# Performance work log

Measured on AMD Instinct MI355X. Metric: run time of the kernel, lower is better.

The kernel has to match this reference:

```python
import jax, jax.numpy as jnp
import numpy as np

B, L, D = 2, 1024, 512
E = 2
DI = E * D            # d_inner = 1024
N = 16                # d_state
K = 4                 # d_conv
DT_RANK = 32          # ceil(d_model / 16)


def setup_inputs() -> dict:
    key = jax.random.key(0)
    ks = jax.random.split(key, 12)
    s = lambda i, shape, scale=0.02: jax.random.normal(ks[i], shape, jnp.float32) * scale
    return {
        "x": jax.random.normal(ks[0], (B, L, D), jnp.float32),
        # Mamba params (mamba_ssm layout: Linear weights are [out, in])
        "W_in": s(1, (2 * DI, D)),                 # in_proj, bias=False
        "conv_w": s(2, (DI, K), 0.1),              # depthwise conv kernel
        "conv_b": jnp.zeros((DI,), jnp.float32),
        "W_xproj": s(3, (DT_RANK + 2 * N, DI)),    # x_proj, bias=False
        "W_dt": s(4, (DI, DT_RANK), 0.1),
        "b_dt": s(5, (DI,), 0.5),
        "A_log": jnp.log(jnp.broadcast_to(jnp.arange(1, N + 1, dtype=jnp.float32), (DI, N))),
        "D_skip": jnp.ones((DI,), jnp.float32),
        "W_out": s(6, (D, DI)),                    # out_proj, bias=False
        # block params
        "g1": jnp.ones((D,), jnp.float32), "b1": jnp.zeros((D,), jnp.float32),
        "W_ff1": s(7, (2 * D, D)), "b_ff1": jnp.zeros((2 * D,), jnp.float32),
        "W_ff2": s(8, (D, 2 * D)), "b_ff2": jnp.zeros((D,), jnp.float32),
        "g2": jnp.ones((D,), jnp.float32), "b2": jnp.zeros((D,), jnp.float32),
    }


def layernorm(x, g, b, eps=1e-5):
    m = x.mean(-1, keepdims=True)
    v = jnp.mean(jnp.square(x - m), -1, keepdims=True)
    return (x - m) * jax.lax.rsqrt(v + eps) * g + b


def mamba(x, W_in, conv_w, conv_b, W_xproj, W_dt, b_dt, A_log, D_skip, W_out):
    xz = x @ W_in.T                              # [B,L,2*DI]
    u, z = jnp.split(xz, 2, axis=-1)             # each [B,L,DI]
    # causal depthwise conv1d over time
    u_t = u.transpose(0, 2, 1)                   # [B,DI,L]
    conv = jax.lax.conv_general_dilated(
        u_t, conv_w[:, None, :], (1,), [(K - 1, 0)], feature_group_count=DI)
    u = jax.nn.silu(conv.transpose(0, 2, 1) + conv_b)   # [B,L,DI]
    # input-dependent dt, B, C
    x_dbl = u @ W_xproj.T                        # [B,L,DT_RANK+2N]
    dt_r, Bm, Cm = jnp.split(x_dbl, [DT_RANK, DT_RANK + N], axis=-1)
    dt = jax.nn.softplus(dt_r @ W_dt.T + b_dt)   # [B,L,DI]
    A = -jnp.exp(A_log)                          # [DI,N]
    dA = jnp.exp(dt[..., None] * A)                                # [B,L,DI,N]
    dBu = dt[..., None] * Bm[:, :, None, :] * u[..., None]         # [B,L,DI,N]

    def step(h, xs):
        dA_t, dBu_t, C_t = xs
        h = dA_t * h + dBu_t                    # [B,DI,N]
        y = jnp.einsum('bdn,bn->bd', h, C_t)
        return h, y

    h0 = jnp.zeros((B, DI, N), dt.dtype)
    _, ys = jax.lax.scan(step, h0, (dA.transpose(1, 0, 2, 3),
                                    dBu.transpose(1, 0, 2, 3),
                                    Cm.transpose(1, 0, 2)))
    y = ys.transpose(1, 0, 2) + u * D_skip       # [B,L,DI]
    y = y * jax.nn.silu(z)
    return y @ W_out.T                            # [B,L,D]


def reference(x, W_in, conv_w, conv_b, W_xproj, W_dt, b_dt, A_log, D_skip, W_out,
              g1, b1, W_ff1, b_ff1, W_ff2, b_ff2, g2, b2):
    m = mamba(x, W_in, conv_w, conv_b, W_xproj, W_dt, b_dt, A_log, D_skip, W_out)
    res1 = x - m
    r = layernorm(res1, g1, b1)
    ff = jax.nn.gelu(r @ W_ff1.T + b_ff1, approximate=False) @ W_ff2.T + b_ff2
    res2 = r - ff
    out = layernorm(jax.nn.silu(res2), g2, b2)
    return out + x
```

## Files before the change

### kernel.cpp

```cpp
#include <hip/hip_runtime.h>
#include <math.h>

#define BB 2
#define LL 1024
#define DD 512
#define DIN 1024
#define NS 16
#define RNK 32
#define ML (BB*LL)
#define CT 16
#define NC (LL/CT)
#define BDIN (BB*DIN)

typedef unsigned short u16;
typedef unsigned int u32;

__device__ __forceinline__ float sigmoidf_(float v) { return 1.f / (1.f + __expf(-v)); }
__device__ __forceinline__ float siluf_(float v) { return v * sigmoidf_(v); }
__device__ __forceinline__ u16 f2bf(float f) {
  union { float f; u32 u; } c; c.f = f;
  u32 r = c.u + 0x7fffu + ((c.u >> 16) & 1u);
  return (u16)(r >> 16);
}
__device__ __forceinline__ float bf2f(u16 x) {
  union { u32 u; float f; } c; c.u = (u32)x << 16;
  return c.f;
}

__global__ __launch_bounds__(256) void cast_all(const float* __restrict__ x,
                                                const float* __restrict__ Wi,
                                                const float* __restrict__ Wx,
                                                const float* __restrict__ Wd,
                                                const float* __restrict__ Wo,
                                                const float* __restrict__ Wf1,
                                                const float* __restrict__ Wf2,
                                                u16* bx, u16* bWi, u16* bWx, u16* bWd,
                                                u16* bWo, u16* bWf1, u16* bWf2)
{
  int bid = blockIdx.x;
  const float* src; u16* dst; int base;
  if (bid < 512)       { src = x;   dst = bx;   base = 0; }
  else if (bid < 1024) { src = Wi;  dst = bWi;  base = 512; }
  else if (bid < 1056) { src = Wx;  dst = bWx;  base = 1024; }
  else if (bid < 1072) { src = Wd;  dst = bWd;  base = 1056; }
  else if (bid < 1328) { src = Wo;  dst = bWo;  base = 1072; }
  else if (bid < 1584) { src = Wf1; dst = bWf1; base = 1328; }
  else                 { src = Wf2; dst = bWf2; base = 1584; }
  int i = ((bid - base) * 256 + threadIdx.x) * 8;
  float4 v0 = *(const float4*)&src[i];
  float4 v1 = *(const float4*)&src[i + 4];
  union { u16 u[8]; uint4 v; } p;
  p.u[0] = f2bf(v0.x); p.u[1] = f2bf(v0.y); p.u[2] = f2bf(v0.z); p.u[3] = f2bf(v0.w);
  p.u[4] = f2bf(v1.x); p.u[5] = f2bf(v1.y); p.u[6] = f2bf(v1.z); p.u[7] = f2bf(v1.w);
  *(uint4*)&dst[i] = p.v;
}

using bf16x8 = __attribute__((ext_vector_type(8))) short;
using f32x4  = __attribute__((ext_vector_type(4))) float;

template<int BM, int BN, int EPI, typename OT>
__global__ __launch_bounds__(256) void gemm_t(const u16* __restrict__ A,
                                              const u16* __restrict__ W,
                                              const float* __restrict__ bias,
                                              OT* __restrict__ C,
                                              int M, int N, int K)
{
  constexpr int WR = BM / 64;
  constexpr int WC = 4 / WR;
  constexpr int NW = BN / WC;
  constexpr int JJ = NW / 16;
  constexpr int RB = BN / 64;
  __shared__ u16 As[BM][40];
  __shared__ u16 Bs[BN][40];
  const int bm = blockIdx.y * BM, bn = blockIdx.x * BN;
  const int tid = threadIdx.x;
  const int w = tid >> 6, l = tid & 63;
  const int wr = w / WC, wc = w % WC;
  const int lr = l & 15, lh = l >> 4;
  const int sr0 = tid >> 2, sc0 = tid & 3;
  f32x4 acc[4][JJ] = {};
  for (int k0 = 0; k0 < K; k0 += 32) {
    uint4 areg[WR], breg[RB];
#pragma unroll
    for (int i = 0; i < WR; ++i)
      areg[i] = *(const uint4*)&A[(size_t)(bm + sr0 + 64 * i) * K + k0 + sc0 * 8];
#pragma unroll
    for (int i = 0; i < RB; ++i)
      breg[i] = *(const uint4*)&W[(size_t)(bn + sr0 + 64 * i) * K + k0 + sc0 * 8];
    __syncthreads();
#pragma unroll
    for (int i = 0; i < WR; ++i) *(uint4*)&As[sr0 + 64 * i][sc0 * 8] = areg[i];
#pragma unroll
    for (int i = 0; i < RB; ++i) *(uint4*)&Bs[sr0 + 64 * i][sc0 * 8] = breg[i];
    __syncthreads();
    bf16x8 af[4], bfr[JJ];
#pragma unroll
    for (int i = 0; i < 4; ++i) af[i]  = *(bf16x8*)&As[wr * 64 + i * 16 + lr][lh * 8];
#pragma unroll
    for (int j = 0; j < JJ; ++j) bfr[j] = *(bf16x8*)&Bs[wc * NW + j * 16 + lr][lh * 8];
#pragma unroll
    for (int i = 0; i < 4; ++i)
#pragma unroll
      for (int j = 0; j < JJ; ++j)
        acc[i][j] = __builtin_amdgcn_mfma_f32_16x16x32_bf16(af[i], bfr[j], acc[i][j], 0, 0, 0);
  }
#pragma unroll
  for (int i = 0; i < 4; ++i) {
#pragma unroll
    for (int j = 0; j < JJ; ++j) {
      int col = bn + wc * NW + j * 16 + lr;
      float bv = (EPI >= 1) ? bias[col] : 0.f;
#pragma unroll
      for (int r = 0; r < 4; ++r) {
        int row = bm + wr * 64 + i * 16 + lh * 4 + r;
        float t = acc[i][j][r] + bv;
        if (EPI == 2) t = 0.5f * t * (1.f + erff(t * 0.70710678118654752f));
        if (EPI == 3) t = fmaxf(t, 0.f) + log1pf(__expf(-fabsf(t)));
        if constexpr (sizeof(OT) == 2) C[(size_t)row * N + col] = (OT)f2bf(t);
        else                           C[(size_t)row * N + col] = (OT)t;
      }
    }
  }
}

__global__ __launch_bounds__(256) void xproj_mfma(const u16* __restrict__ A,
                                                  const u16* __restrict__ W,
                                                  float* __restrict__ C,
                                                  u16* __restrict__ bdtr)
{
  __shared__ u16 As[128][40];
  __shared__ u16 Bs[64][40];
  const int bm = blockIdx.x * 128;
  const int tid = threadIdx.x;
  const int w = tid >> 6, l = tid & 63;
  const int lr = l & 15, lh = l >> 4;
  const int sr0 = tid >> 2, sc0 = tid & 3;
  f32x4 acc[2][4] = {};
  for (int k0 = 0; k0 < DIN; k0 += 32) {
    uint4 a0 = *(const uint4*)&A[(size_t)(bm + sr0) * DIN + k0 + sc0 * 8];
    uint4 a1 = *(const uint4*)&A[(size_t)(bm + sr0 + 64) * DIN + k0 + sc0 * 8];
    uint4 b0;
    if (sr0 < 64) b0 = *(const uint4*)&W[(size_t)sr0 * DIN + k0 + sc0 * 8];
    __syncthreads();
    *(uint4*)&As[sr0][sc0 * 8] = a0;
    *(uint4*)&As[sr0 + 64][sc0 * 8] = a1;
    if (sr0 < 64) *(uint4*)&Bs[sr0][sc0 * 8] = b0;
    __syncthreads();
    bf16x8 af[2], bfr[4];
#pragma unroll
    for (int i = 0; i < 2; ++i) af[i]  = *(bf16x8*)&As[w * 32 + i * 16 + lr][lh * 8];
#pragma unroll
    for (int j = 0; j < 4; ++j) bfr[j] = *(bf16x8*)&Bs[j * 16 + lr][lh * 8];
#pragma unroll
    for (int i = 0; i < 2; ++i)
#pragma unroll
      for (int j = 0; j < 4; ++j)
        acc[i][j] = __builtin_amdgcn_mfma_f32_16x16x32_bf16(af[i], bfr[j], acc[i][j], 0, 0, 0);
  }
#pragma unroll
  for (int i = 0; i < 2; ++i)
#pragma unroll
    for (int j = 0; j < 4; ++j) {
      int col = j * 16 + lr;
#pragma unroll
      for (int r = 0; r < 4; ++r) {
        int row = bm + w * 32 + i * 16 + lh * 4 + r;
        float v = acc[i][j][r];
        C[(size_t)row * 64 + col] = v;
        if (j < 2) bdtr[(size_t)row * RNK + col] = f2bf(v);
      }
    }
}

__global__ __launch_bounds__(256) void conv_silu(const u16* __restrict__ xzb,
                                                 const float* __restrict__ conv_w,
                                                 const float* __restrict__ conv_b,
                                                 u16* __restrict__ ucb)
{
  int idx = blockIdx.x * 256 + threadIdx.x;
  int d = idx & (DIN - 1);
  int bl = idx >> 10;
  int l = bl & (LL - 1);
  int b = bl >> 10;
  float acc = conv_b[d];
#pragma unroll
  for (int k = 0; k < 4; ++k) {
    int ls = l - 3 + k;
    float uv = (ls >= 0) ? bf2f(xzb[((size_t)(b * LL + ls)) * (2 * DIN) + d]) : 0.f;
    acc = fmaf(uv, conv_w[d * 4 + k], acc);
  }
  ucb[idx] = f2bf(siluf_(acc));
}


__global__ __launch_bounds__(256) void scan_p1(const float* __restrict__ dt,
                                               const u16* __restrict__ ucb,
                                               const float* __restrict__ xdbl,
                                               const float* __restrict__ A_log,
                                               float* __restrict__ apG,
                                               float* __restrict__ hG)
{
  __shared__ float dts[CT][256];
  __shared__ float us[CT][256];
  __shared__ float Bs[CT][NS];
  const int d0 = blockIdx.x * 256, c = blockIdx.y, b = blockIdx.z;
  const int tid = threadIdx.x;
  const int t0 = c * CT;
  for (int i = tid; i < CT * 64; i += 256) {
    int r = i >> 6, col = (i & 63) * 4;
    size_t row = (size_t)(b * LL + t0 + r);
    *(float4*)&dts[r][col] = *(const float4*)&dt[row * DIN + d0 + col];
    ushort4 uv = *(const ushort4*)&ucb[row * DIN + d0 + col];
    float4 uf = { bf2f(uv.x), bf2f(uv.y), bf2f(uv.z), bf2f(uv.w) };
    *(float4*)&us[r][col] = uf;
  }
  { int r = tid >> 4, n = tid & 15;
    Bs[r][n] = xdbl[(size_t)(b * LL + t0 + r) * 64 + 32 + n]; }
  __syncthreads();
  const int d = d0 + tid;
  float Ad[NS];
#pragma unroll
  for (int n = 0; n < NS; ++n) Ad[n] = -__expf(A_log[d * NS + n]);
  float h[NS] = {};
  float sdt = 0.f;
#pragma unroll 4
  for (int t = 0; t < CT; ++t) {
    float dtv = dts[t][tid];
    float dtu = dtv * us[t][tid];
    sdt += dtv;
    float4 B0 = *(float4*)&Bs[t][0],  B1 = *(float4*)&Bs[t][4];
    float4 B2 = *(float4*)&Bs[t][8],  B3 = *(float4*)&Bs[t][12];
    float Bq[NS] = { B0.x, B0.y, B0.z, B0.w, B1.x, B1.y, B1.z, B1.w,
                     B2.x, B2.y, B2.z, B2.w, B3.x, B3.y, B3.z, B3.w };
#pragma unroll
    for (int n = 0; n < NS; ++n) {
      float a = __expf(dtv * Ad[n]);
      h[n] = fmaf(a, h[n], dtu * Bq[n]);
    }
  }
  const int bd = b * DIN + d;
#pragma unroll
  for (int n = 0; n < NS; ++n) {
    apG[((size_t)c * NS + n) * BDIN + bd] = __expf(Ad[n] * sdt);
    hG [((size_t)c * NS + n) * BDIN + bd] = h[n];
  }
}

__global__ __launch_bounds__(128) void scan_p2(const float* __restrict__ apG,
                                               float* __restrict__ hG)
{
  const int idx = blockIdx.x * 128 + threadIdx.x;
  float H = 0.f;
#pragma unroll 16
  for (int c = 0; c < NC; ++c) {
    size_t o = (size_t)c * (NS * BDIN) + idx;
    float ap = apG[o];
    float hl = hG[o];
    hG[o] = H;
    H = fmaf(ap, H, hl);
  }
}

__global__ __launch_bounds__(256) void scan_p3(const float* __restrict__ dt,
                                               const u16* __restrict__ ucb,
                                               const u16* __restrict__ xzb,
                                               const float* __restrict__ xdbl,
                                               const float* __restrict__ A_log,
                                               const float* __restrict__ D_skip,
                                               const float* __restrict__ hG,
                                               u16* __restrict__ ygb)
{
  __shared__ float dts[CT][256];
  __shared__ float us[CT][256];
  __shared__ float zs[CT][256];
  __shared__ float Bs[CT][NS];
  __shared__ float Cs[CT][NS];
  const int d0 = blockIdx.x * 256, c = blockIdx.y, b = blockIdx.z;
  const int tid = threadIdx.x;
  const int t0 = c * CT;
  for (int i = tid; i < CT * 64; i += 256) {
    int r = i >> 6, col = (i & 63) * 4;
    size_t row = (size_t)(b * LL + t0 + r);
    *(float4*)&dts[r][col] = *(const float4*)&dt[row * DIN + d0 + col];
    ushort4 uv = *(const ushort4*)&ucb[row * DIN + d0 + col];
    float4 uf = { bf2f(uv.x), bf2f(uv.y), bf2f(uv.z), bf2f(uv.w) };
    *(float4*)&us[r][col] = uf;
    ushort4 zv = *(const ushort4*)&xzb[row * (2 * DIN) + DIN + d0 + col];
    float4 zf = { bf2f(zv.x), bf2f(zv.y), bf2f(zv.z), bf2f(zv.w) };
    *(float4*)&zs[r][col] = zf;
  }
  { int r = tid >> 4, n = tid & 15;
    size_t row = (size_t)(b * LL + t0 + r);
    Bs[r][n] = xdbl[row * 64 + 32 + n];
    Cs[r][n] = xdbl[row * 64 + 48 + n]; }
  __syncthreads();
  const int d = d0 + tid;
  const int bd = b * DIN + d;
  float Ad[NS];
#pragma unroll
  for (int n = 0; n < NS; ++n) Ad[n] = -__expf(A_log[d * NS + n]);
  const float Dd = D_skip[d];
  float h[NS];
#pragma unroll
  for (int n = 0; n < NS; ++n) h[n] = hG[((size_t)c * NS + n) * BDIN + bd];
#pragma unroll 2
  for (int t = 0; t < CT; ++t) {
    float dtv = dts[t][tid];
    float ucv = us[t][tid];
    float dtu = dtv * ucv;
    float4 B0 = *(float4*)&Bs[t][0],  B1 = *(float4*)&Bs[t][4];
    float4 B2 = *(float4*)&Bs[t][8],  B3 = *(float4*)&Bs[t][12];
    float4 C0 = *(float4*)&Cs[t][0],  C1 = *(float4*)&Cs[t][4];
    float4 C2 = *(float4*)&Cs[t][8],  C3 = *(float4*)&Cs[t][12];
    float Bq[NS] = { B0.x, B0.y, B0.z, B0.w, B1.x, B1.y, B1.z, B1.w,
                     B2.x, B2.y, B2.z, B2.w, B3.x, B3.y, B3.z, B3.w };
    float Cq[NS] = { C0.x, C0.y, C0.z, C0.w, C1.x, C1.y, C1.z, C1.w,
                     C2.x, C2.y, C2.z, C2.w, C3.x, C3.y, C3.z, C3.w };
    float y = 0.f;
#pragma unroll
    for (int n = 0; n < NS; ++n) {
      float a = __expf(dtv * Ad[n]);
      h[n] = fmaf(a, h[n], dtu * Bq[n]);
      y = fmaf(h[n], Cq[n], y);
    }
    float o = fmaf(ucv, Dd, y) * siluf_(zs[t][tid]);
    ygb[(size_t)(b * LL + t0 + t) * DIN + d0 + tid] = f2bf(o);
  }
}

__global__ __launch_bounds__(256) void ln1_kernel(const float* __restrict__ x,
                                                  const float* __restrict__ m,
                                                  const float* __restrict__ g,
                                                  const float* __restrict__ b,
                                                  float* __restrict__ r,
                                                  u16* __restrict__ rbf)
{
  int row = blockIdx.x;
  int tid = threadIdx.x;
  size_t base = (size_t)row * DD;
  float2 xv = *(const float2*)&x[base + tid * 2];
  float2 mv = *(const float2*)&m[base + tid * 2];
  float v0 = xv.x - mv.x, v1 = xv.y - mv.y;
  float s = v0 + v1, ss = v0 * v0 + v1 * v1;
#pragma unroll
  for (int off = 32; off; off >>= 1) { s += __shfl_down(s, off, 64); ss += __shfl_down(ss, off, 64); }
  __shared__ float sm[8];
  int w = tid >> 6;
  if ((tid & 63) == 0) { sm[w] = s; sm[4 + w] = ss; }
  __syncthreads();
  float S = sm[0] + sm[1] + sm[2] + sm[3];
  float SS = sm[4] + sm[5] + sm[6] + sm[7];
  float mean = S * (1.f / DD);
  float var = SS * (1.f / DD) - mean * mean;
  float rstd = rsqrtf(var + 1e-5f);
  float2 gv = *(const float2*)&g[tid * 2];
  float2 bv = *(const float2*)&b[tid * 2];
  float2 o;
  o.x = (v0 - mean) * rstd * gv.x + bv.x;
  o.y = (v1 - mean) * rstd * gv.y + bv.y;
  *(float2*)&r[base + tid * 2] = o;
  u32 pk = (u32)f2bf(o.x) | ((u32)f2bf(o.y) << 16);
  *(u32*)&rbf[base + tid * 2] = pk;
}

__global__ __launch_bounds__(256) void final_kernel(const float* __restrict__ r,
                                                    const float* __restrict__ ff,
                                                    const float* __restrict__ x,
                                                    const float* __restrict__ g,
                                                    const float* __restrict__ b,
                                                    float* __restrict__ out)
{
  int row = blockIdx.x;
  int tid = threadIdx.x;
  size_t base = (size_t)row * DD;
  float2 rv = *(const float2*)&r[base + tid * 2];
  float2 fv = *(const float2*)&ff[base + tid * 2];
  float v0 = rv.x - fv.x, v1 = rv.y - fv.y;
  v0 = siluf_(v0); v1 = siluf_(v1);
  float s = v0 + v1, ss = v0 * v0 + v1 * v1;
#pragma unroll
  for (int off = 32; off; off >>= 1) { s += __shfl_down(s, off, 64); ss += __shfl_down(ss, off, 64); }
  __shared__ float sm[8];
  int w = tid >> 6;
  if ((tid & 63) == 0) { sm[w] = s; sm[4 + w] = ss; }
  __syncthreads();
  float S = sm[0] + sm[1] + sm[2] + sm[3];
  float SS = sm[4] + sm[5] + sm[6] + sm[7];
  float mean = S * (1.f / DD);
  float var = SS * (1.f / DD) - mean * mean;
  float rstd = rsqrtf(var + 1e-5f);
  float2 gv = *(const float2*)&g[tid * 2];
  float2 bv = *(const float2*)&b[tid * 2];
  float2 xv = *(const float2*)&x[base + tid * 2];
  float2 o;
  o.x = (v0 - mean) * rstd * gv.x + bv.x + xv.x;
  o.y = (v1 - mean) * rstd * gv.y + bv.y + xv.y;
  *(float2*)&out[base + tid * 2] = o;
}

extern "C" void kernel_launch(void* const* d_in, const int* in_sizes, int n_in,
                              void* d_out, int out_size, void* d_ws, size_t ws_size,
                              hipStream_t stream)
{
  const float* x      = (const float*)d_in[0];
  const float* W_in   = (const float*)d_in[1];
  const float* conv_w = (const float*)d_in[2];
  const float* conv_b = (const float*)d_in[3];
  const float* W_xp   = (const float*)d_in[4];
  const float* W_dt   = (const float*)d_in[5];
  const float* b_dt   = (const float*)d_in[6];
  const float* A_log  = (const float*)d_in[7];
  const float* D_skip = (const float*)d_in[8];
  const float* W_out  = (const float*)d_in[9];
  const float* g1     = (const float*)d_in[10];
  const float* b1     = (const float*)d_in[11];
  const float* W_ff1  = (const float*)d_in[12];
  const float* b_ff1  = (const float*)d_in[13];
  const float* W_ff2  = (const float*)d_in[14];
  const float* b_ff2  = (const float*)d_in[15];
  const float* g2     = (const float*)d_in[16];
  const float* b2     = (const float*)d_in[17];
  float* out = (float*)d_out;

  float* ws = (float*)d_ws;
  u16*   xzb    = (u16*)ws;
  float* xdbl   = ws + 4194304;
  float* dtb    = ws + 4325376;
  float* apG    = ws + 6422528;
  float* hG     = ws + 8519680;
  float* mb     = ws + 10616832;
  float* rb     = ws + 11665408;
  u16*   bffh   = (u16*)(ws + 12713984);
  u16*   ygb    = (u16*)(ws + 13762560);
  u16*   ucb    = (u16*)(ws + 14811136);
  u16*   brb    = (u16*)(ws + 15859712);
  u16*   bdtr   = (u16*)(ws + 16384000);
  u16*   bx     = (u16*)(ws + 16416768);
  u16*   bW_in  = (u16*)(ws + 16941056);
  u16*   bWxp   = (u16*)(ws + 17989632);
  u16*   bW_dt  = (u16*)(ws + 18022400);
  u16*   bW_out = (u16*)(ws + 18038784);
  u16*   bW_ff1 = (u16*)(ws + 18300928);
  u16*   bW_ff2 = (u16*)(ws + 18563072);

  cast_all<<<1840, 256, 0, stream>>>(x, W_in, W_xp, W_dt, W_out, W_ff1, W_ff2,
                                     bx, bW_in, bWxp, bW_dt, bW_out, bW_ff1, bW_ff2);
  gemm_t<128, 64, 0, u16><<<dim3(2 * DIN / 64, ML / 128), 256, 0, stream>>>(
      bx, bW_in, nullptr, xzb, ML, 2 * DIN, DD);
  conv_silu<<<(ML * DIN) / 256, 256, 0, stream>>>(xzb, conv_w, conv_b, ucb);
  xproj_mfma<<<ML / 128, 256, 0, stream>>>(ucb, bWxp, xdbl, bdtr);
  gemm_t<128, 64, 3, float><<<dim3(DIN / 64, ML / 128), 256, 0, stream>>>(
      bdtr, bW_dt, b_dt, dtb, ML, DIN, RNK);
  scan_p1<<<dim3(DIN / 256, NC, BB), 256, 0, stream>>>(dtb, ucb, xdbl, A_log, apG, hG);
  scan_p2<<<(NS * BDIN) / 128, 128, 0, stream>>>(apG, hG);
  scan_p3<<<dim3(DIN / 256, NC, BB), 256, 0, stream>>>(dtb, ucb, xzb, xdbl, A_log, D_skip,
                                                       hG, ygb);
  gemm_t<64, 64, 0, float><<<dim3(DD / 64, ML / 64), 256, 0, stream>>>(
      ygb, bW_out, nullptr, mb, ML, DD, DIN);
  ln1_kernel<<<ML, 256, 0, stream>>>(x, mb, g1, b1, rb, brb);
  gemm_t<128, 64, 2, u16><<<dim3(DIN / 64, ML / 128), 256, 0, stream>>>(
      brb, bW_ff1, b_ff1, bffh, ML, DIN, DD);
  gemm_t<64, 64, 1, float><<<dim3(DD / 64, ML / 64), 256, 0, stream>>>(
      bffh, bW_ff2, b_ff2, mb, ML, DD, DIN);
  final_kernel<<<ML, 256, 0, stream>>>(rb, mb, x, g2, b2, out);
}
```

Before: 174.0 us.

## Fuse out_proj and FF2 GEMMs with layernorm epilogues; store dt as bf16

Replaces the out_proj GEMM plus ln1 kernel and the FF2 GEMM plus final kernel with a single full-row GEMM kernel (64 rows x 512 cols per block) that computes the residual, layernorm statistics via shuffles and shared memory, and writes normalized output directly. This removes the intermediate fp32 buffer round trips and two launches. It also stores dt in bf16 to halve its traffic in the scan kernels. The fused GEMM launches only 32 blocks, which risks severe underutilization of the GPU, and bf16 dt reduces precision.

After: 351.4 us. 102% more time.

```diff
diff --git a/kernel.cpp b/kernel.cpp
--- a/kernel.cpp
+++ b/kernel.cpp
@@ -123,6 +123,110 @@
   }
 }
 
+template<int MODE>
+__global__ __launch_bounds__(256) void gemm_ln(const u16* __restrict__ A,
+                                               const u16* __restrict__ W,
+                                               const float* __restrict__ bias,
+                                               const float* __restrict__ xres,
+                                               const float* __restrict__ rln,
+                                               const float* __restrict__ g,
+                                               const float* __restrict__ b,
+                                               float* __restrict__ outF,
+                                               u16* __restrict__ outB)
+{
+  constexpr int K = DIN;
+  __shared__ u16 As[64][40];
+  __shared__ u16 Bs[512][40];
+  __shared__ float red[64][8];
+  const int bm = blockIdx.x * 64;
+  const int tid = threadIdx.x;
+  const int wv = tid >> 6, l = tid & 63;
+  const int lr = l & 15, lh = l >> 4;
+  const int sr0 = tid >> 2, sc0 = tid & 3;
+  f32x4 acc[4][8] = {};
+  for (int k0 = 0; k0 < K; k0 += 32) {
+    uint4 areg = *(const uint4*)&A[(size_t)(bm + sr0) * K + k0 + sc0 * 8];
+    uint4 breg[8];
+#pragma unroll
+    for (int i = 0; i < 8; ++i)
+      breg[i] = *(const uint4*)&W[(size_t)(sr0 + 64 * i) * K + k0 + sc0 * 8];
+    __syncthreads();
+    *(uint4*)&As[sr0][sc0 * 8] = areg;
+#pragma unroll
+    for (int i = 0; i < 8; ++i) *(uint4*)&Bs[sr0 + 64 * i][sc0 * 8] = breg[i];
+    __syncthreads();
+    bf16x8 af[4], bfr[8];
+#pragma unroll
+    for (int i = 0; i < 4; ++i) af[i]  = *(bf16x8*)&As[i * 16 + lr][lh * 8];
+#pragma unroll
+    for (int j = 0; j < 8; ++j) bfr[j] = *(bf16x8*)&Bs[wv * 128 + j * 16 + lr][lh * 8];
+#pragma unroll
+    for (int i = 0; i < 4; ++i)
+#pragma unroll
+      for (int j = 0; j < 8; ++j)
+        acc[i][j] = __builtin_amdgcn_mfma_f32_16x16x32_bf16(af[i], bfr[j], acc[i][j], 0, 0, 0);
+  }
+#pragma unroll
+  for (int i = 0; i < 4; ++i)
+#pragma unroll
+    for (int j = 0; j < 8; ++j) {
+      int col = wv * 128 + j * 16 + lr;
+#pragma unroll
+      for (int r = 0; r < 4; ++r) {
+        int row = bm + i * 16 + lh * 4 + r;
+        float a = acc[i][j][r];
+        float v;
+        if (MODE == 0) {
+          v = xres[(size_t)row * DD + col] - a;
+        } else {
+          float ff = a + bias[col];
+          v = siluf_(rln[(size_t)row * DD + col] - ff);
+        }
+        acc[i][j][r] = v;
+      }
+    }
+#pragma unroll
+  for (int i = 0; i < 4; ++i)
+#pragma unroll
+    for (int r = 0; r < 4; ++r) {
+      float s = 0.f, ss = 0.f;
+#pragma unroll
+      for (int j = 0; j < 8; ++j) {
+        float v = acc[i][j][r];
+        s += v; ss += v * v;
+      }
+      s  += __shfl_xor(s, 1, 16);  ss += __shfl_xor(ss, 1, 16);
+      s  += __shfl_xor(s, 2, 16);  ss += __shfl_xor(ss, 2, 16);
+      s  += __shfl_xor(s, 4, 16);  ss += __shfl_xor(ss, 4, 16);
+      s  += __shfl_xor(s, 8, 16);  ss += __shfl_xor(ss, 8, 16);
+      if (lr == 0) { red[i * 16 + lh * 4 + r][wv * 2] = s; red[i * 16 + lh * 4 + r][wv * 2 + 1] = ss; }
+    }
+  __syncthreads();
+#pragma unroll
+  for (int i = 0; i < 4; ++i)
+#pragma unroll
+    for (int r = 0; r < 4; ++r) {
+      int rlcl = i * 16 + lh * 4 + r;
+      int row = bm + rlcl;
+      float S  = red[rlcl][0] + red[rlcl][2] + red[rlcl][4] + red[rlcl][6];
+      float SS = red[rlcl][1] + red[rlcl][3] + red[rlcl][5] + red[rlcl][7];
+      float mean = S * (1.f / DD);
+      float var = SS * (1.f / DD) - mean * mean;
+      float rstd = rsqrtf(var + 1e-5f);
+#pragma unroll
+      for (int j = 0; j < 8; ++j) {
+        int col = wv * 128 + j * 16 + lr;
+        float vn = (acc[i][j][r] - mean) * rstd * g[col] + b[col];
+        if (MODE == 0) {
+          outF[(size_t)row * DD + col] = vn;
+          outB[(size_t)row * DD + col] = f2bf(vn);
+        } else {
+          outF[(size_t)row * DD + col] = vn + xres[(size_t)row * DD + col];
+        }
+      }
+    }
+}
+
 __global__ __launch_bounds__(256) void xproj_mfma(const u16* __restrict__ A,
                                                   const u16* __restrict__ W,
                                                   float* __restrict__ C,
@@ -193,7 +297,7 @@
 }
 
 
-__global__ __launch_bounds__(256) void scan_p1(const float* __restrict__ dt,
+__global__ __launch_bounds__(256) void scan_p1(const u16* __restrict__ dtb,
                                                const u16* __restrict__ ucb,
                                                const float* __restrict__ xdbl,
                                                const float* __restrict__ A_log,
@@ -209,7 +313,9 @@
   for (int i = tid; i < CT * 64; i += 256) {
     int r = i >> 6, col = (i & 63) * 4;
     size_t row = (size_t)(b * LL + t0 + r);
-    *(float4*)&dts[r][col] = *(const float4*)&dt[row * DIN + d0 + col];
+    ushort4 dv = *(const ushort4*)&dtb[row * DIN + d0 + col];
+    float4 df = { bf2f(dv.x), bf2f(dv.y), bf2f(dv.z), bf2f(dv.w) };
+    *(float4*)&dts[r][col] = df;
     ushort4 uv = *(const ushort4*)&ucb[row * DIN + d0 + col];
     float4 uf = { bf2f(uv.x), bf2f(uv.y), bf2f(uv.z), bf2f(uv.w) };
     *(float4*)&us[r][col] = uf;
@@ -261,7 +367,7 @@
   }
 }
 
-__global__ __launch_bounds__(256) void scan_p3(const float* __restrict__ dt,
+__global__ __launch_bounds__(256) void scan_p3(const u16* __restrict__ dtb,
                                                const u16* __restrict__ ucb,
                                                const u16* __restrict__ xzb,
                                                const float* __restrict__ xdbl,
@@ -281,7 +387,9 @@
   for (int i = tid; i < CT * 64; i += 256) {
     int r = i >> 6, col = (i & 63) * 4;
     size_t row = (size_t)(b * LL + t0 + r);
-    *(float4*)&dts[r][col] = *(const float4*)&dt[row * DIN + d0 + col];
+    ushort4 dv = *(const ushort4*)&dtb[row * DIN + d0 + col];
+    float4 df = { bf2f(dv.x), bf2f(dv.y), bf2f(dv.z), bf2f(dv.w) };
+    *(float4*)&dts[r][col] = df;
     ushort4 uv = *(const ushort4*)&ucb[row * DIN + d0 + col];
     float4 uf = { bf2f(uv.x), bf2f(uv.y), bf2f(uv.z), bf2f(uv.w) };
     *(float4*)&us[r][col] = uf;
@@ -326,76 +434,6 @@
     float o = fmaf(ucv, Dd, y) * siluf_(zs[t][tid]);
     ygb[(size_t)(b * LL + t0 + t) * DIN + d0 + tid] = f2bf(o);
   }
-}
-
-__global__ __launch_bounds__(256) void ln1_kernel(const float* __restrict__ x,
-                                                  const float* __restrict__ m,
-                                                  const float* __restrict__ g,
-                                                  const float* __restrict__ b,
-                                                  float* __restrict__ r,
-                                                  u16* __restrict__ rbf)
-{
-  int row = blockIdx.x;
-  int tid = threadIdx.x;
-  size_t base = (size_t)row * DD;
-  float2 xv = *(const float2*)&x[base + tid * 2];
-  float2 mv = *(const float2*)&m[base + tid * 2];
-  float v0 = xv.x - mv.x, v1 = xv.y - mv.y;
-  float s = v0 + v1, ss = v0 * v0 + v1 * v1;
-#pragma unroll
-  for (int off = 32; off; off >>= 1) { s += __shfl_down(s, off, 64); ss += __shfl_down(ss, off, 64); }
-  __shared__ float sm[8];
-  int w = tid >> 6;
-  if ((tid & 63) == 0) { sm[w] = s; sm[4 + w] = ss; }
-  __syncthreads();
-  float S = sm[0] + sm[1] + sm[2] + sm[3];
-  float SS = sm[4] + sm[5] + sm[6] + sm[7];
-  float mean = S * (1.f / DD);
-  float var = SS * (1.f / DD) - mean * mean;
-  float rstd = rsqrtf(var + 1e-5f);
-  float2 gv = *(const float2*)&g[tid * 2];
-  float2 bv = *(const float2*)&b[tid * 2];
-  float2 o;
-  o.x = (v0 - mean) * rstd * gv.x + bv.x;
-  o.y = (v1 - mean) * rstd * gv.y + bv.y;
-  *(float2*)&r[base + tid * 2] = o;
-  u32 pk = (u32)f2bf(o.x) | ((u32)f2bf(o.y) << 16);
-  *(u32*)&rbf[base + tid * 2] = pk;
-}
-
-__global__ __launch_bounds__(256) void final_kernel(const float* __restrict__ r,
-                                                    const float* __restrict__ ff,
-                                                    const float* __restrict__ x,
-                                                    const float* __restrict__ g,
-                                                    const float* __restrict__ b,
-                                                    float* __restrict__ out)
-{
-  int row = blockIdx.x;
-  int tid = threadIdx.x;
-  size_t base = (size_t)row * DD;
-  float2 rv = *(const float2*)&r[base + tid * 2];
-  float2 fv = *(const float2*)&ff[base + tid * 2];
-  float v0 = rv.x - fv.x, v1 = rv.y - fv.y;
-  v0 = siluf_(v0); v1 = siluf_(v1);
-  float s = v0 + v1, ss = v0 * v0 + v1 * v1;
-#pragma unroll
-  for (int off = 32; off; off >>= 1) { s += __shfl_down(s, off, 64); ss += __shfl_down(ss, off, 64); }
-  __shared__ float sm[8];
-  int w = tid >> 6;
-  if ((tid & 63) == 0) { sm[w] = s; sm[4 + w] = ss; }
-  __syncthreads();
-  float S = sm[0] + sm[1] + sm[2] + sm[3];
-  float SS = sm[4] + sm[5] + sm[6] + sm[7];
-  float mean = S * (1.f / DD);
-  float var = SS * (1.f / DD) - mean * mean;
-  float rstd = rsqrtf(var + 1e-5f);
-  float2 gv = *(const float2*)&g[tid * 2];
-  float2 bv = *(const float2*)&b[tid * 2];
-  float2 xv = *(const float2*)&x[base + tid * 2];
-  float2 o;
-  o.x = (v0 - mean) * rstd * gv.x + bv.x + xv.x;
-  o.y = (v1 - mean) * rstd * gv.y + bv.y + xv.y;
-  *(float2*)&out[base + tid * 2] = o;
 }
 
 extern "C" void kernel_launch(void* const* d_in, const int* in_sizes, int n_in,
@@ -425,10 +463,9 @@
   float* ws = (float*)d_ws;
   u16*   xzb    = (u16*)ws;
   float* xdbl   = ws + 4194304;
-  float* dtb    = ws + 4325376;
+  u16*   dtb    = (u16*)(ws + 4325376);
   float* apG    = ws + 6422528;
   float* hG     = ws + 8519680;
-  float* mb     = ws + 10616832;
   float* rb     = ws + 11665408;
   u16*   bffh   = (u16*)(ws + 12713984);
   u16*   ygb    = (u16*)(ws + 13762560);
@@ -449,18 +486,14 @@
       bx, bW_in, nullptr, xzb, ML, 2 * DIN, DD);
   conv_silu<<<(ML * DIN) / 256, 256, 0, stream>>>(xzb, conv_w, conv_b, ucb);
   xproj_mfma<<<ML / 128, 256, 0, stream>>>(ucb, bWxp, xdbl, bdtr);
-  gemm_t<128, 64, 3, float><<<dim3(DIN / 64, ML / 128), 256, 0, stream>>>(
+  gemm_t<128, 64, 3, u16><<<dim3(DIN / 64, ML / 128), 256, 0, stream>>>(
       bdtr, bW_dt, b_dt, dtb, ML, DIN, RNK);
   scan_p1<<<dim3(DIN / 256, NC, BB), 256, 0, stream>>>(dtb, ucb, xdbl, A_log, apG, hG);
   scan_p2<<<(NS * BDIN) / 128, 128, 0, stream>>>(apG, hG);
   scan_p3<<<dim3(DIN / 256, NC, BB), 256, 0, stream>>>(dtb, ucb, xzb, xdbl, A_log, D_skip,
                                                        hG, ygb);
-  gemm_t<64, 64, 0, float><<<dim3(DD / 64, ML / 64), 256, 0, stream>>>(
-      ygb, bW_out, nullptr, mb, ML, DD, DIN);
-  ln1_kernel<<<ML, 256, 0, stream>>>(x, mb, g1, b1, rb, brb);
+  gemm_ln<0><<<ML / 64, 256, 0, stream>>>(ygb, bW_out, nullptr, x, nullptr, g1, b1, rb, brb);
   gemm_t<128, 64, 2, u16><<<dim3(DIN / 64, ML / 128), 256, 0, stream>>>(
       brb, bW_ff1, b_ff1, bffh, ML, DIN, DD);
-  gemm_t<64, 64, 1, float><<<dim3(DD / 64, ML / 64), 256, 0, stream>>>(
-      bffh, bW_ff2, b_ff2, mb, ML, DD, DIN);
-  final_kernel<<<ML, 256, 0, stream>>>(rb, mb, x, g2, b2, out);
-}
+  gemm_ln<1><<<ML / 64, 256, 0, stream>>>(bffh, bW_ff2, b_ff2, x, rb, g2, b2, out, nullptr);
+}
```

## Fuse fp32-to-bf16 casts into GEMM loads and store dt as bf16

Applied to the files above, without the earlier changes.

Removes the standalone cast_all kernel and converts x and the weights from fp32 to bf16 inside each GEMM's global load path through a templated ld8bf helper. The dt softplus output is now stored as bf16 rather than fp32, so the scan kernels read half as many bytes for dt. This saves a kernel launch and a write/read round trip for the casted buffers. In exchange, weights are re-read as fp32 and re-converted by every block tile that touches them, and dt loses precision.

Result: no change. 174.9 us (+0.5%).

```diff
diff --git a/kernel.cpp b/kernel.cpp
--- a/kernel.cpp
+++ b/kernel.cpp
@@ -27,40 +27,26 @@
   return c.f;
 }
 
-__global__ __launch_bounds__(256) void cast_all(const float* __restrict__ x,
-                                                const float* __restrict__ Wi,
-                                                const float* __restrict__ Wx,
-                                                const float* __restrict__ Wd,
-                                                const float* __restrict__ Wo,
-                                                const float* __restrict__ Wf1,
-                                                const float* __restrict__ Wf2,
-                                                u16* bx, u16* bWi, u16* bWx, u16* bWd,
-                                                u16* bWo, u16* bWf1, u16* bWf2)
-{
-  int bid = blockIdx.x;
-  const float* src; u16* dst; int base;
-  if (bid < 512)       { src = x;   dst = bx;   base = 0; }
-  else if (bid < 1024) { src = Wi;  dst = bWi;  base = 512; }
-  else if (bid < 1056) { src = Wx;  dst = bWx;  base = 1024; }
-  else if (bid < 1072) { src = Wd;  dst = bWd;  base = 1056; }
-  else if (bid < 1328) { src = Wo;  dst = bWo;  base = 1072; }
-  else if (bid < 1584) { src = Wf1; dst = bWf1; base = 1328; }
-  else                 { src = Wf2; dst = bWf2; base = 1584; }
-  int i = ((bid - base) * 256 + threadIdx.x) * 8;
-  float4 v0 = *(const float4*)&src[i];
-  float4 v1 = *(const float4*)&src[i + 4];
-  union { u16 u[8]; uint4 v; } p;
-  p.u[0] = f2bf(v0.x); p.u[1] = f2bf(v0.y); p.u[2] = f2bf(v0.z); p.u[3] = f2bf(v0.w);
-  p.u[4] = f2bf(v1.x); p.u[5] = f2bf(v1.y); p.u[6] = f2bf(v1.z); p.u[7] = f2bf(v1.w);
-  *(uint4*)&dst[i] = p.v;
+template<typename T>
+__device__ __forceinline__ uint4 ld8bf(const T* p);
+template<> __device__ __forceinline__ uint4 ld8bf<u16>(const u16* p) {
+  return *(const uint4*)p;
+}
+template<> __device__ __forceinline__ uint4 ld8bf<float>(const float* p) {
+  float4 v0 = *(const float4*)p;
+  float4 v1 = *(const float4*)(p + 4);
+  union { u16 u[8]; uint4 v; } q;
+  q.u[0] = f2bf(v0.x); q.u[1] = f2bf(v0.y); q.u[2] = f2bf(v0.z); q.u[3] = f2bf(v0.w);
+  q.u[4] = f2bf(v1.x); q.u[5] = f2bf(v1.y); q.u[6] = f2bf(v1.z); q.u[7] = f2bf(v1.w);
+  return q.v;
 }
 
 using bf16x8 = __attribute__((ext_vector_type(8))) short;
 using f32x4  = __attribute__((ext_vector_type(4))) float;
 
-template<int BM, int BN, int EPI, typename OT>
-__global__ __launch_bounds__(256) void gemm_t(const u16* __restrict__ A,
-                                              const u16* __restrict__ W,
+template<int BM, int BN, int EPI, typename OT, typename TA, typename TW>
+__global__ __launch_bounds__(256) void gemm_t(const TA* __restrict__ A,
+                                              const TW* __restrict__ W,
                                               const float* __restrict__ bias,
                                               OT* __restrict__ C,
                                               int M, int N, int K)
@@ -83,10 +69,10 @@
     uint4 areg[WR], breg[RB];
 #pragma unroll
     for (int i = 0; i < WR; ++i)
-      areg[i] = *(const uint4*)&A[(size_t)(bm + sr0 + 64 * i) * K + k0 + sc0 * 8];
+      areg[i] = ld8bf(&A[(size_t)(bm + sr0 + 64 * i) * K + k0 + sc0 * 8]);
 #pragma unroll
     for (int i = 0; i < RB; ++i)
-      breg[i] = *(const uint4*)&W[(size_t)(bn + sr0 + 64 * i) * K + k0 + sc0 * 8];
+      breg[i] = ld8bf(&W[(size_t)(bn + sr0 + 64 * i) * K + k0 + sc0 * 8]);
     __syncthreads();
 #pragma unroll
     for (int i = 0; i < WR; ++i) *(uint4*)&As[sr0 + 64 * i][sc0 * 8] = areg[i];
@@ -124,7 +110,7 @@
 }
 
 __global__ __launch_bounds__(256) void xproj_mfma(const u16* __restrict__ A,
-                                                  const u16* __restrict__ W,
+                                                  const float* __restrict__ W,
                                                   float* __restrict__ C,
                                                   u16* __restrict__ bdtr)
 {
@@ -137,10 +123,10 @@
   const int sr0 = tid >> 2, sc0 = tid & 3;
   f32x4 acc[2][4] = {};
   for (int k0 = 0; k0 < DIN; k0 += 32) {
-    uint4 a0 = *(const uint4*)&A[(size_t)(bm + sr0) * DIN + k0 + sc0 * 8];
-    uint4 a1 = *(const uint4*)&A[(size_t)(bm + sr0 + 64) * DIN + k0 + sc0 * 8];
+    uint4 a0 = ld8bf(&A[(size_t)(bm + sr0) * DIN + k0 + sc0 * 8]);
+    uint4 a1 = ld8bf(&A[(size_t)(bm + sr0 + 64) * DIN + k0 + sc0 * 8]);
     uint4 b0;
-    if (sr0 < 64) b0 = *(const uint4*)&W[(size_t)sr0 * DIN + k0 + sc0 * 8];
+    if (sr0 < 64) b0 = ld8bf(&W[(size_t)sr0 * DIN + k0 + sc0 * 8]);
     __syncthreads();
     *(uint4*)&As[sr0][sc0 * 8] = a0;
     *(uint4*)&As[sr0 + 64][sc0 * 8] = a1;
@@ -193,7 +179,7 @@
 }
 
 
-__global__ __launch_bounds__(256) void scan_p1(const float* __restrict__ dt,
+__global__ __launch_bounds__(256) void scan_p1(const u16* __restrict__ dtb,
                                                const u16* __restrict__ ucb,
                                                const float* __restrict__ xdbl,
                                                const float* __restrict__ A_log,
@@ -209,7 +195,9 @@
   for (int i = tid; i < CT * 64; i += 256) {
     int r = i >> 6, col = (i & 63) * 4;
     size_t row = (size_t)(b * LL + t0 + r);
-    *(float4*)&dts[r][col] = *(const float4*)&dt[row * DIN + d0 + col];
+    ushort4 dv = *(const ushort4*)&dtb[row * DIN + d0 + col];
+    float4 df = { bf2f(dv.x), bf2f(dv.y), bf2f(dv.z), bf2f(dv.w) };
+    *(float4*)&dts[r][col] = df;
     ushort4 uv = *(const ushort4*)&ucb[row * DIN + d0 + col];
     float4 uf = { bf2f(uv.x), bf2f(uv.y), bf2f(uv.z), bf2f(uv.w) };
     *(float4*)&us[r][col] = uf;
@@ -261,7 +249,7 @@
   }
 }
 
-__global__ __launch_bounds__(256) void scan_p3(const float* __restrict__ dt,
+__global__ __launch_bounds__(256) void scan_p3(const u16* __restrict__ dtb,
                                                const u16* __restrict__ ucb,
                                                const u16* __restrict__ xzb,
                                                const float* __restrict__ xdbl,
@@ -281,7 +269,9 @@
   for (int i = tid; i < CT * 64; i += 256) {
     int r = i >> 6, col = (i & 63) * 4;
     size_t row = (size_t)(b * LL + t0 + r);
-    *(float4*)&dts[r][col] = *(const float4*)&dt[row * DIN + d0 + col];
+    ushort4 dv = *(const ushort4*)&dtb[row * DIN + d0 + col];
+    float4 df = { bf2f(dv.x), bf2f(dv.y), bf2f(dv.z), bf2f(dv.w) };
+    *(float4*)&dts[r][col] = df;
     ushort4 uv = *(const ushort4*)&ucb[row * DIN + d0 + col];
     float4 uf = { bf2f(uv.x), bf2f(uv.y), bf2f(uv.z), bf2f(uv.w) };
     *(float4*)&us[r][col] = uf;
@@ -423,44 +413,35 @@
   float* out = (float*)d_out;
 
   float* ws = (float*)d_ws;
-  u16*   xzb    = (u16*)ws;
-  float* xdbl   = ws + 4194304;
-  float* dtb    = ws + 4325376;
-  float* apG    = ws + 6422528;
-  float* hG     = ws + 8519680;
-  float* mb     = ws + 10616832;
-  float* rb     = ws + 11665408;
-  u16*   bffh   = (u16*)(ws + 12713984);
-  u16*   ygb    = (u16*)(ws + 13762560);
-  u16*   ucb    = (u16*)(ws + 14811136);
-  u16*   brb    = (u16*)(ws + 15859712);
-  u16*   bdtr   = (u16*)(ws + 16384000);
-  u16*   bx     = (u16*)(ws + 16416768);
-  u16*   bW_in  = (u16*)(ws + 16941056);
-  u16*   bWxp   = (u16*)(ws + 17989632);
-  u16*   bW_dt  = (u16*)(ws + 18022400);
-  u16*   bW_out = (u16*)(ws + 18038784);
-  u16*   bW_ff1 = (u16*)(ws + 18300928);
-  u16*   bW_ff2 = (u16*)(ws + 18563072);
-
-  cast_all<<<1840, 256, 0, stream>>>(x, W_in, W_xp, W_dt, W_out, W_ff1, W_ff2,
-                                     bx, bW_in, bWxp, bW_dt, bW_out, bW_ff1, bW_ff2);
-  gemm_t<128, 64, 0, u16><<<dim3(2 * DIN / 64, ML / 128), 256, 0, stream>>>(
-      bx, bW_in, nullptr, xzb, ML, 2 * DIN, DD);
+  u16*   xzb  = (u16*)ws;
+  float* xdbl = ws + 2097152;
+  u16*   dtb  = (u16*)(ws + 2228224);
+  float* apG  = ws + 3276800;
+  float* hG   = ws + 5373952;
+  float* mb   = ws + 7471104;
+  float* rb   = ws + 8519680;
+  u16*   bffh = (u16*)(ws + 9568256);
+  u16*   ygb  = (u16*)(ws + 10616832);
+  u16*   ucb  = (u16*)(ws + 11665408);
+  u16*   brb  = (u16*)(ws + 12713984);
+  u16*   bdtr = (u16*)(ws + 13238272);
+
+  gemm_t<128, 64, 0, u16, float, float><<<dim3(2 * DIN / 64, ML / 128), 256, 0, stream>>>(
+      x, W_in, nullptr, xzb, ML, 2 * DIN, DD);
   conv_silu<<<(ML * DIN) / 256, 256, 0, stream>>>(xzb, conv_w, conv_b, ucb);
-  xproj_mfma<<<ML / 128, 256, 0, stream>>>(ucb, bWxp, xdbl, bdtr);
-  gemm_t<128, 64, 3, float><<<dim3(DIN / 64, ML / 128), 256, 0, stream>>>(
-      bdtr, bW_dt, b_dt, dtb, ML, DIN, RNK);
+  xproj_mfma<<<ML / 128, 256, 0, stream>>>(ucb, W_xp, xdbl, bdtr);
+  gemm_t<128, 64, 3, u16, u16, float><<<dim3(DIN / 64, ML / 128), 256, 0, stream>>>(
+      bdtr, W_dt, b_dt, dtb, ML, DIN, RNK);
   scan_p1<<<dim3(DIN / 256, NC, BB), 256, 0, stream>>>(dtb, ucb, xdbl, A_log, apG, hG);
   scan_p2<<<(NS * BDIN) / 128, 128, 0, stream>>>(apG, hG);
   scan_p3<<<dim3(DIN / 256, NC, BB), 256, 0, stream>>>(dtb, ucb, xzb, xdbl, A_log, D_skip,
                                                        hG, ygb);
-  gemm_t<64, 64, 0, float><<<dim3(DD / 64, ML / 64), 256, 0, stream>>>(
-      ygb, bW_out, nullptr, mb, ML, DD, DIN);
+  gemm_t<64, 64, 0, float, u16, float><<<dim3(DD / 64, ML / 64), 256, 0, stream>>>(
+      ygb, W_out, nullptr, mb, ML, DD, DIN);
   ln1_kernel<<<ML, 256, 0, stream>>>(x, mb, g1, b1, rb, brb);
-  gemm_t<128, 64, 2, u16><<<dim3(DIN / 64, ML / 128), 256, 0, stream>>>(
-      brb, bW_ff1, b_ff1, bffh, ML, DIN, DD);
-  gemm_t<64, 64, 1, float><<<dim3(DD / 64, ML / 64), 256, 0, stream>>>(
-      bffh, bW_ff2, b_ff2, mb, ML, DD, DIN);
+  gemm_t<128, 64, 2, u16, u16, float><<<dim3(DIN / 64, ML / 128), 256, 0, stream>>>(
+      brb, W_ff1, b_ff1, bffh, ML, DIN, DD);
+  gemm_t<64, 64, 1, float, u16, float><<<dim3(DD / 64, ML / 64), 256, 0, stream>>>(
+      bffh, W_ff2, b_ff2, mb, ML, DD, DIN);
   final_kernel<<<ML, 256, 0, stream>>>(rb, mb, x, g2, b2, out);
 }
```
